# Kernel tuning notes

Measured on AMD Instinct MI355X. Metric: run time of the kernel, lower is better.

Reference implementation:

```python
import jax, jax.numpy as jnp
import numpy as np

N = 50000
H = 4
C = 32  # hidden_channels // heads
NEG_SLOPE = 0.2


def gat_layer(x, W, a_src, a_dst, b, src, dst):
    # x: [N, F_in]; W: [F_in, H*C]; a_src/a_dst: [H, C]; b: [H*C]
    h = (x @ W).reshape(N, H, C)                      # [N, H, C]
    alpha_src = jnp.sum(h * a_src, axis=-1)           # [N, H]
    alpha_dst = jnp.sum(h * a_dst, axis=-1)           # [N, H]
    e = jax.nn.leaky_relu(alpha_src[src] + alpha_dst[dst], NEG_SLOPE)  # [E, H]
    # softmax over incoming edges per destination node (stable)
    m = jax.ops.segment_max(e, dst, num_segments=N)   # [N, H]
    p = jnp.exp(e - m[dst])                           # [E, H]
    s = jax.ops.segment_sum(p, dst, num_segments=N)   # [N, H]
    alpha = p / s[dst]                                # [E, H]
    msg = h[src] * alpha[:, :, None]                  # [E, H, C]
    out = jax.ops.segment_sum(msg, dst, num_segments=N)  # [N, H, C]
    return out.reshape(N, H * C) + b


def setup_inputs() -> dict:
    key = jax.random.key(0)
    ks = jax.random.split(key, 12)
    E = 1600000
    x = jax.random.normal(ks[0], (N, 128), dtype=jnp.float32)
    edge_index = jax.random.randint(ks[1], (2, E), 0, N, dtype=jnp.int32)
    s = 0.08
    return {
        "x": x,
        "edge_index": edge_index,
        "W1": jax.random.normal(ks[2], (128, H * C), dtype=jnp.float32) * s,
        "a_src1": jax.random.normal(ks[3], (H, C), dtype=jnp.float32) * s,
        "a_dst1": jax.random.normal(ks[4], (H, C), dtype=jnp.float32) * s,
        "b1": jnp.zeros((H * C,), dtype=jnp.float32),
        "W2": jax.random.normal(ks[5], (H * C, H * C), dtype=jnp.float32) * s,
        "a_src2": jax.random.normal(ks[6], (H, C), dtype=jnp.float32) * s,
        "a_dst2": jax.random.normal(ks[7], (H, C), dtype=jnp.float32) * s,
        "b2": jnp.zeros((H * C,), dtype=jnp.float32),
    }


def reference(x, edge_index, W1, a_src1, a_dst1, b1, W2, a_src2, a_dst2, b2):
    # PyG GATConv default add_self_loops=True: append (i -> i) edges
    loops = jnp.arange(N, dtype=edge_index.dtype)
    src = jnp.concatenate([edge_index[0], loops])
    dst = jnp.concatenate([edge_index[1], loops])
    # layer 1 + ELU (dropout is identity in eval mode)
    h = gat_layer(x, W1, a_src1, a_dst1, b1, src, dst)
    h = jax.nn.elu(h)
    # layer 2 + ELU
    h = gat_layer(h, W2, a_src2, a_dst2, b2, src, dst)
    h = jax.nn.elu(h)
    return h
```

## Files before the change

### kernel.cpp

```cpp
#include <hip/hip_runtime.h>
#include <hip/hip_bf16.h>

static __device__ __forceinline__ float bf2f_lo(unsigned u) {
    return __uint_as_float(u << 16);
}
static __device__ __forceinline__ float bf2f_hi(unsigned u) {
    return __uint_as_float(u & 0xffff0000u);
}
static __device__ __forceinline__ unsigned f2bf_rne_bits(float f) {
    unsigned u = __float_as_uint(f);
    return u + 0x7fffu + ((u >> 16) & 1u);
}
static __device__ __forceinline__ unsigned pack_bf2(float a, float b) {
    return (f2bf_rne_bits(a) >> 16) | (f2bf_rne_bits(b) & 0xffff0000u);
}
static __device__ __forceinline__ float pfun(float e) {
    e = fmaxf(e, 0.2f * e);
    return __expf(e);
}

#define CHUNK 4096

__global__ void kb_zero(int* bucketCount, int NBK) {
    int i = blockIdx.x * 256 + threadIdx.x;
    if (i < NBK) bucketCount[i] = 0;
}

__global__ void kb_count(const int* __restrict__ dst, int* bucketCount,
                         int E, int T, int NBK) {
    __shared__ int cnt[256];
    const int tid = threadIdx.x;
    const int beg = blockIdx.x * CHUNK;
    const int end = min(beg + CHUNK, T);
    cnt[tid] = 0;
    __syncthreads();
    for (int i = beg + tid; i < end; i += 256) {
        int d = (i < E) ? dst[i] : (i - E);
        atomicAdd(&cnt[d >> 8], 1);
    }
    __syncthreads();
    if (tid < NBK && cnt[tid] > 0) atomicAdd(&bucketCount[tid], cnt[tid]);
}

__global__ void kb_scan(const int* __restrict__ bucketCount, int* bucketBase,
                        int* bucketCursor, int* row_ptr, int NBK, int N, int total) {
    __shared__ int sm[256];
    const int tid = threadIdx.x;
    int v = (tid < NBK) ? bucketCount[tid] : 0;
    sm[tid] = v;
    __syncthreads();
    for (int off = 1; off < 256; off <<= 1) {
        int t = (tid >= off) ? sm[tid - off] : 0;
        __syncthreads();
        sm[tid] += t;
        __syncthreads();
    }
    if (tid < NBK) {
        int ex = sm[tid] - v;
        bucketBase[tid] = ex;
        bucketCursor[tid] = ex;
    }
    if (tid == 0) {
        bucketBase[NBK] = total;
        row_ptr[N] = total;
    }
}

__global__ void kb_place(const int* __restrict__ src, const int* __restrict__ dst,
                         int* bucketCursor, unsigned* __restrict__ barr,
                         int E, int T, int NBK) {
    __shared__ int cnt[256];
    __shared__ int wb[256];
    const int tid = threadIdx.x;
    const int beg = blockIdx.x * CHUNK;
    const int end = min(beg + CHUNK, T);
    cnt[tid] = 0;
    __syncthreads();
    for (int i = beg + tid; i < end; i += 256) {
        int d = (i < E) ? dst[i] : (i - E);
        atomicAdd(&cnt[d >> 8], 1);
    }
    __syncthreads();
    if (tid < NBK) {
        int c = cnt[tid];
        wb[tid] = (c > 0) ? atomicAdd(&bucketCursor[tid], c) : 0;
    }
    __syncthreads();
    cnt[tid] = 0;
    __syncthreads();
    for (int i = beg + tid; i < end; i += 256) {
        int s, d;
        if (i < E) { s = src[i]; d = dst[i]; }
        else       { s = i - E;  d = s; }
        int g = d >> 8;
        unsigned pk = (unsigned)s | ((unsigned)(d & 255) << 16);
        int r = atomicAdd(&cnt[g], 1);
        barr[wb[g] + r] = pk;
    }
}

__global__ void kb_csr(const unsigned* __restrict__ barr, const int* __restrict__ bucketBase,
                       int* __restrict__ row_ptr, int* __restrict__ col, int N) {
    __shared__ int cnt[256];
    __shared__ int sm[256];
    __shared__ int cur[256];
    const int tid = threadIdx.x;
    const int b = blockIdx.x;
    const int beg = bucketBase[b];
    const int end = bucketBase[b + 1];
    cnt[tid] = 0;
    __syncthreads();
    for (int i = beg + tid; i < end; i += 256)
        atomicAdd(&cnt[barr[i] >> 16], 1);
    __syncthreads();
    int v = cnt[tid];
    sm[tid] = v;
    __syncthreads();
    for (int off = 1; off < 256; off <<= 1) {
        int t = (tid >= off) ? sm[tid - off] : 0;
        __syncthreads();
        sm[tid] += t;
        __syncthreads();
    }
    int ex = sm[tid] - v;
    int n = b * 256 + tid;
    if (n < N) row_ptr[n] = beg + ex;
    cur[tid] = beg + ex;
    __syncthreads();
    for (int i = beg + tid; i < end; i += 256) {
        unsigned p = barr[i];
        int pos = atomicAdd(&cur[p >> 16], 1);
        col[pos] = (int)(p & 0xFFFFu);
    }
}

#define KC 32
__launch_bounds__(512, 1)
__global__ void k_gemm(const float* __restrict__ A, const float* __restrict__ W,
                       const float* __restrict__ a_src, const float* __restrict__ a_dst,
                       unsigned* __restrict__ Hout,
                       float* __restrict__ asrc_o, float* __restrict__ adst_o,
                       int nrows) {
    __shared__ float Wl[KC * 128];
    __shared__ float Xl[128 * (KC + 4)];
    const int tid = threadIdx.x;
    const int tx = tid & 15;
    const int ty = tid >> 4;
    const int row0 = blockIdx.x * 128;

    float acc[4][8];
#pragma unroll
    for (int i = 0; i < 4; i++)
#pragma unroll
        for (int j = 0; j < 8; j++) acc[i][j] = 0.f;

    for (int kc = 0; kc < 128; kc += KC) {
#pragma unroll
        for (int it = 0; it < 2; ++it) {
            int ff = it * 512 + tid;
            int r = ff >> 5, cq = ff & 31;
            *(float4*)&Wl[r * 128 + cq * 4] = *(const float4*)&W[(size_t)(kc + r) * 128 + cq * 4];
        }
#pragma unroll
        for (int it = 0; it < 2; ++it) {
            int ff = it * 512 + tid;
            int r = ff >> 3, kq = ff & 7;
            int gr = row0 + r;
            float4 v = make_float4(0.f, 0.f, 0.f, 0.f);
            if (gr < nrows) v = *(const float4*)&A[(size_t)gr * 128 + kc + kq * 4];
            *(float4*)&Xl[r * (KC + 4) + kq * 4] = v;
        }
        __syncthreads();
#pragma unroll
        for (int k0 = 0; k0 < KC; k0 += 4) {
            float4 xv[4];
#pragma unroll
            for (int i = 0; i < 4; i++)
                xv[i] = *(float4*)&Xl[(4 * ty + i) * (KC + 4) + k0];
            const float* xp = (const float*)xv;
#pragma unroll
            for (int kk = 0; kk < 4; ++kk) {
                float4 w0 = *(float4*)&Wl[(k0 + kk) * 128 + 8 * tx];
                float4 w1 = *(float4*)&Wl[(k0 + kk) * 128 + 8 * tx + 4];
#pragma unroll
                for (int i = 0; i < 4; i++) {
                    float xs = xp[i * 4 + kk];
                    acc[i][0] += xs * w0.x; acc[i][1] += xs * w0.y;
                    acc[i][2] += xs * w0.z; acc[i][3] += xs * w0.w;
                    acc[i][4] += xs * w1.x; acc[i][5] += xs * w1.y;
                    acc[i][6] += xs * w1.z; acc[i][7] += xs * w1.w;
                }
            }
        }
        __syncthreads();
    }

    const int head = tx >> 2;
    const int c0 = 8 * tx;
    float as_c[8], ad_c[8];
#pragma unroll
    for (int j = 0; j < 8; j++) { as_c[j] = a_src[c0 + j]; ad_c[j] = a_dst[c0 + j]; }
#pragma unroll
    for (int i = 0; i < 4; i++) {
        int gr = row0 + 4 * ty + i;
        float ps = 0.f, pd = 0.f;
#pragma unroll
        for (int j = 0; j < 8; j++) { ps += acc[i][j] * as_c[j]; pd += acc[i][j] * ad_c[j]; }
        ps += __shfl_xor(ps, 1); ps += __shfl_xor(ps, 2);
        pd += __shfl_xor(pd, 1); pd += __shfl_xor(pd, 2);
        if (gr < nrows) {
            if ((tx & 3) == 0) {
                asrc_o[(size_t)gr * 4 + head] = ps;
                adst_o[(size_t)gr * 4 + head] = pd;
            }
            uint4 o;
            o.x = pack_bf2(acc[i][0], acc[i][1]);
            o.y = pack_bf2(acc[i][2], acc[i][3]);
            o.z = pack_bf2(acc[i][4], acc[i][5]);
            o.w = pack_bf2(acc[i][6], acc[i][7]);
            *(uint4*)&Hout[(size_t)gr * 64 + 4 * tx] = o;
        }
    }
}

#define BAT 16
__launch_bounds__(256)
__global__ void k_aggr(const unsigned* __restrict__ h,
                       const float* __restrict__ asrc, const float* __restrict__ adst,
                       const float* __restrict__ bias,
                       const int* __restrict__ row_ptr, const int* __restrict__ col,
                       float* __restrict__ out, int N) {
    const int lane = threadIdx.x & 63;
    const int d = blockIdx.x * 4 + (threadIdx.x >> 6);
    if (d >= N) return;
    const int eb  = lane >> 2;
    const int hp  = lane & 3;
    const int hdc = lane >> 4;
    const float adv = adst[(size_t)d * 4 + hp];
    const int beg = row_ptr[d];
    const int end = row_ptr[d + 1];

    float ac0 = 0.f, ac1 = 0.f, sp = 0.f;

    int cv = 0;
    { int idx = beg + eb; if (idx < end) cv = col[idx]; }

    for (int j = beg; j < end; j += BAT) {
        int cvn = 0;
        { int idx = j + BAT + eb; if (idx < end) cvn = col[idx]; }

        float a = asrc[(size_t)(unsigned)cv * 4 + hp];
        float p = (j + eb < end) ? pfun(a + adv) : 0.f;
        sp += p;

        unsigned u[BAT];
#pragma unroll
        for (int k = 0; k < BAT; ++k) {
            int sk = __builtin_amdgcn_readlane(cv, 4 * k);
            u[k] = h[(size_t)(unsigned)sk * 64 + lane];
        }
#pragma unroll
        for (int k = 0; k < BAT; ++k) {
            float pk = __shfl(p, 4 * k + hdc);
            ac0 += pk * bf2f_lo(u[k]);
            ac1 += pk * bf2f_hi(u[k]);
        }
        cv = cvn;
    }

    sp += __shfl_xor(sp, 4);
    sp += __shfl_xor(sp, 8);
    sp += __shfl_xor(sp, 16);
    sp += __shfl_xor(sp, 32);
    float spv = __shfl(sp, hdc);
    float inv = 1.f / spv;

    int c = 2 * lane;
    float v0 = ac0 * inv + bias[c];
    float v1 = ac1 * inv + bias[c + 1];
    v0 = (v0 > 0.f) ? v0 : (__expf(v0) - 1.f);
    v1 = (v1 > 0.f) ? v1 : (__expf(v1) - 1.f);
    *(float2*)&out[(size_t)d * 128 + c] = make_float2(v0, v1);
}

extern "C" void kernel_launch(void* const* d_in, const int* in_sizes, int n_in,
                              void* d_out, int out_size, void* d_ws, size_t ws_size,
                              hipStream_t stream) {
    const float* x      = (const float*)d_in[0];
    const int*   ei     = (const int*)d_in[1];
    const float* W1     = (const float*)d_in[2];
    const float* a_src1 = (const float*)d_in[3];
    const float* a_dst1 = (const float*)d_in[4];
    const float* b1     = (const float*)d_in[5];
    const float* W2     = (const float*)d_in[6];
    const float* a_src2 = (const float*)d_in[7];
    const float* a_dst2 = (const float*)d_in[8];
    const float* b2     = (const float*)d_in[9];

    const int N = in_sizes[0] / 128;
    const int E = in_sizes[1] / 2;
    const int T = E + N;
    const int NBK = (N + 255) / 256;
    const int* src = ei;
    const int* dst = ei + E;

    char* w = (char*)d_ws;
    auto alloc = [&](size_t bytes) -> char* {
        char* p = w;
        w += (bytes + 255) & ~(size_t)255;
        return p;
    };
    unsigned* h_bf    = (unsigned*)alloc((size_t)N * 64 * 4);
    float*    o1      = (float*)alloc((size_t)N * 128 * 4);
    float*    asrc    = (float*)alloc((size_t)N * 4 * 4);
    float*    adst    = (float*)alloc((size_t)N * 4 * 4);
    int*      row_ptr = (int*)alloc((size_t)(N + 1) * 4);
    int*      col     = (int*)alloc((size_t)T * 4);
    int*      bCount  = (int*)alloc((size_t)NBK * 4);
    int*      bBase   = (int*)alloc((size_t)(NBK + 1) * 4);
    int*      bCursor = (int*)alloc((size_t)NBK * 4);
    unsigned* barr    = (unsigned*)o1;
    (void)ws_size; (void)n_in; (void)out_size;

    const int PB = (T + CHUNK - 1) / CHUNK;

    hipLaunchKernelGGL(kb_zero, dim3((NBK + 255) / 256), dim3(256), 0, stream, bCount, NBK);
    hipLaunchKernelGGL(kb_count, dim3(PB), dim3(256), 0, stream, dst, bCount, E, T, NBK);
    hipLaunchKernelGGL(kb_scan, dim3(1), dim3(256), 0, stream, bCount, bBase, bCursor, row_ptr, NBK, N, T);
    hipLaunchKernelGGL(kb_place, dim3(PB), dim3(256), 0, stream, src, dst, bCursor, barr, E, T, NBK);
    hipLaunchKernelGGL(kb_csr, dim3(NBK), dim3(256), 0, stream, barr, bBase, row_ptr, col, N);

    const int GB = (N + 127) / 128;
    const int AB = (N + 3) / 4;

    hipLaunchKernelGGL(k_gemm, dim3(GB), dim3(512), 0, stream, x, W1, a_src1, a_dst1, h_bf, asrc, adst, N);
    hipLaunchKernelGGL(k_aggr, dim3(AB), dim3(256), 0, stream, h_bf, asrc, adst, b1, row_ptr, col, o1, N);
    hipLaunchKernelGGL(k_gemm, dim3(GB), dim3(512), 0, stream, o1, W2, a_src2, a_dst2, h_bf, asrc, adst, N);
    hipLaunchKernelGGL(k_aggr, dim3(AB), dim3(256), 0, stream, h_bf, asrc, adst, b2, row_ptr, col, (float*)d_out, N);
}
```

Before: 329.2 us.

## Rewrite node projection GEMM with fp16 MFMA and persistent waves

Replaces the fp32 SIMT tiled GEMM with a kernel that converts W to fp16 once per block, keeps the weight fragments in registers, and runs 16x16x32 f16 MFMA instructions over 16-row tiles in a persistent grid-stride loop. Attention logits are computed from the MFMA accumulators with cross-lane shuffles. The aim is to cut the GEMM's ALU cost and its shared-memory staging. It gives up precision by converting inputs and weights to fp16, and the large register-resident weight set may limit occupancy.

New measurement: 307.0 us. -6.7%, faster.

```diff
diff --git a/kernel.cpp b/kernel.cpp
--- a/kernel.cpp
+++ b/kernel.cpp
@@ -1,5 +1,8 @@
 #include <hip/hip_runtime.h>
 #include <hip/hip_bf16.h>
+
+typedef _Float16 half8 __attribute__((ext_vector_type(8)));
+typedef float f32x4 __attribute__((ext_vector_type(4)));
 
 static __device__ __forceinline__ float bf2f_lo(unsigned u) {
     return __uint_as_float(u << 16);
@@ -134,91 +137,84 @@
     }
 }
 
-#define KC 32
-__launch_bounds__(512, 1)
+__launch_bounds__(256)
 __global__ void k_gemm(const float* __restrict__ A, const float* __restrict__ W,
                        const float* __restrict__ a_src, const float* __restrict__ a_dst,
                        unsigned* __restrict__ Hout,
                        float* __restrict__ asrc_o, float* __restrict__ adst_o,
-                       int nrows) {
-    __shared__ float Wl[KC * 128];
-    __shared__ float Xl[128 * (KC + 4)];
-    const int tid = threadIdx.x;
-    const int tx = tid & 15;
-    const int ty = tid >> 4;
-    const int row0 = blockIdx.x * 128;
-
-    float acc[4][8];
-#pragma unroll
-    for (int i = 0; i < 4; i++)
-#pragma unroll
-        for (int j = 0; j < 8; j++) acc[i][j] = 0.f;
-
-    for (int kc = 0; kc < 128; kc += KC) {
-#pragma unroll
-        for (int it = 0; it < 2; ++it) {
-            int ff = it * 512 + tid;
-            int r = ff >> 5, cq = ff & 31;
-            *(float4*)&Wl[r * 128 + cq * 4] = *(const float4*)&W[(size_t)(kc + r) * 128 + cq * 4];
-        }
-#pragma unroll
-        for (int it = 0; it < 2; ++it) {
-            int ff = it * 512 + tid;
-            int r = ff >> 3, kq = ff & 7;
-            int gr = row0 + r;
-            float4 v = make_float4(0.f, 0.f, 0.f, 0.f);
-            if (gr < nrows) v = *(const float4*)&A[(size_t)gr * 128 + kc + kq * 4];
-            *(float4*)&Xl[r * (KC + 4) + kq * 4] = v;
-        }
-        __syncthreads();
-#pragma unroll
-        for (int k0 = 0; k0 < KC; k0 += 4) {
-            float4 xv[4];
-#pragma unroll
-            for (int i = 0; i < 4; i++)
-                xv[i] = *(float4*)&Xl[(4 * ty + i) * (KC + 4) + k0];
-            const float* xp = (const float*)xv;
-#pragma unroll
-            for (int kk = 0; kk < 4; ++kk) {
-                float4 w0 = *(float4*)&Wl[(k0 + kk) * 128 + 8 * tx];
-                float4 w1 = *(float4*)&Wl[(k0 + kk) * 128 + 8 * tx + 4];
-#pragma unroll
-                for (int i = 0; i < 4; i++) {
-                    float xs = xp[i * 4 + kk];
-                    acc[i][0] += xs * w0.x; acc[i][1] += xs * w0.y;
-                    acc[i][2] += xs * w0.z; acc[i][3] += xs * w0.w;
-                    acc[i][4] += xs * w1.x; acc[i][5] += xs * w1.y;
-                    acc[i][6] += xs * w1.z; acc[i][7] += xs * w1.w;
-                }
+                       int nrows, int ntiles) {
+    __shared__ _Float16 Wt[128 * 136];
+    const int tid = threadIdx.x;
+    for (int idx = tid; idx < 128 * 128 / 4; idx += 256) {
+        int k = idx >> 5;
+        int c4 = (idx & 31) * 4;
+        float4 v = *(const float4*)&W[(size_t)k * 128 + c4];
+        Wt[(c4 + 0) * 136 + k] = (_Float16)v.x;
+        Wt[(c4 + 1) * 136 + k] = (_Float16)v.y;
+        Wt[(c4 + 2) * 136 + k] = (_Float16)v.z;
+        Wt[(c4 + 3) * 136 + k] = (_Float16)v.w;
+    }
+    __syncthreads();
+    const int lane = tid & 63;
+    const int m = lane & 15, quad = lane >> 4;
+
+    half8 wf[4][8];
+#pragma unroll
+    for (int ks = 0; ks < 4; ++ks)
+#pragma unroll
+        for (int ct = 0; ct < 8; ++ct)
+            wf[ks][ct] = *(half8*)&Wt[(ct * 16 + m) * 136 + ks * 32 + quad * 8];
+
+    const int wv = (blockIdx.x * 256 + tid) >> 6;
+    const int nwaves = gridDim.x * 4;
+    for (int t = wv; t < ntiles; t += nwaves) {
+        const int row = t * 16 + m;
+        const int rc = min(row, nrows - 1);
+        const float* ap = A + (size_t)rc * 128;
+        f32x4 acc[8];
+#pragma unroll
+        for (int ct = 0; ct < 8; ++ct) acc[ct] = (f32x4){0.f, 0.f, 0.f, 0.f};
+#pragma unroll
+        for (int ks = 0; ks < 4; ++ks) {
+            float4 x0 = *(const float4*)&ap[ks * 32 + quad * 8];
+            float4 x1 = *(const float4*)&ap[ks * 32 + quad * 8 + 4];
+            half8 af;
+            af[0] = (_Float16)x0.x; af[1] = (_Float16)x0.y;
+            af[2] = (_Float16)x0.z; af[3] = (_Float16)x0.w;
+            af[4] = (_Float16)x1.x; af[5] = (_Float16)x1.y;
+            af[6] = (_Float16)x1.z; af[7] = (_Float16)x1.w;
+#pragma unroll
+            for (int ct = 0; ct < 8; ++ct)
+                acc[ct] = __builtin_amdgcn_mfma_f32_16x16x32_f16(wf[ks][ct], af, acc[ct], 0, 0, 0);
+        }
+        if (row < nrows) {
+#pragma unroll
+            for (int ct = 0; ct < 8; ++ct) {
+                uint2 o;
+                o.x = pack_bf2(acc[ct][0], acc[ct][1]);
+                o.y = pack_bf2(acc[ct][2], acc[ct][3]);
+                *(uint2*)&Hout[(size_t)row * 64 + ct * 8 + quad * 2] = o;
             }
         }
-        __syncthreads();
-    }
-
-    const int head = tx >> 2;
-    const int c0 = 8 * tx;
-    float as_c[8], ad_c[8];
-#pragma unroll
-    for (int j = 0; j < 8; j++) { as_c[j] = a_src[c0 + j]; ad_c[j] = a_dst[c0 + j]; }
-#pragma unroll
-    for (int i = 0; i < 4; i++) {
-        int gr = row0 + 4 * ty + i;
-        float ps = 0.f, pd = 0.f;
-#pragma unroll
-        for (int j = 0; j < 8; j++) { ps += acc[i][j] * as_c[j]; pd += acc[i][j] * ad_c[j]; }
-        ps += __shfl_xor(ps, 1); ps += __shfl_xor(ps, 2);
-        pd += __shfl_xor(pd, 1); pd += __shfl_xor(pd, 2);
-        if (gr < nrows) {
-            if ((tx & 3) == 0) {
-                asrc_o[(size_t)gr * 4 + head] = ps;
-                adst_o[(size_t)gr * 4 + head] = pd;
+        float ps[4] = {0.f, 0.f, 0.f, 0.f}, pd[4] = {0.f, 0.f, 0.f, 0.f};
+#pragma unroll
+        for (int ct = 0; ct < 8; ++ct) {
+            int hh = ct >> 1;
+#pragma unroll
+            for (int r = 0; r < 4; ++r) {
+                int c = ct * 16 + quad * 4 + r;
+                ps[hh] += acc[ct][r] * a_src[c];
+                pd[hh] += acc[ct][r] * a_dst[c];
             }
-            uint4 o;
-            o.x = pack_bf2(acc[i][0], acc[i][1]);
-            o.y = pack_bf2(acc[i][2], acc[i][3]);
-            o.z = pack_bf2(acc[i][4], acc[i][5]);
-            o.w = pack_bf2(acc[i][6], acc[i][7]);
-            *(uint4*)&Hout[(size_t)gr * 64 + 4 * tx] = o;
+        }
+#pragma unroll
+        for (int hh = 0; hh < 4; ++hh) {
+            ps[hh] += __shfl_xor(ps[hh], 16); ps[hh] += __shfl_xor(ps[hh], 32);
+            pd[hh] += __shfl_xor(pd[hh], 16); pd[hh] += __shfl_xor(pd[hh], 32);
+        }
+        if (row < nrows) {
+            asrc_o[(size_t)row * 4 + quad] = ps[quad];
+            adst_o[(size_t)row * 4 + quad] = pd[quad];
         }
     }
 }
@@ -241,7 +237,6 @@
     const int end = row_ptr[d + 1];
 
     float ac0 = 0.f, ac1 = 0.f, sp = 0.f;
-
     int cv = 0;
     { int idx = beg + eb; if (idx < end) cv = col[idx]; }
 
@@ -330,11 +325,12 @@
     hipLaunchKernelGGL(kb_place, dim3(PB), dim3(256), 0, stream, src, dst, bCursor, barr, E, T, NBK);
     hipLaunchKernelGGL(kb_csr, dim3(NBK), dim3(256), 0, stream, barr, bBase, row_ptr, col, N);
 
-    const int GB = (N + 127) / 128;
+    const int ntiles = (N + 15) / 16;
+    const int GB = 512;
     const int AB = (N + 3) / 4;
 
-    hipLaunchKernelGGL(k_gemm, dim3(GB), dim3(512), 0, stream, x, W1, a_src1, a_dst1, h_bf, asrc, adst, N);
+    hipLaunchKernelGGL(k_gemm, dim3(GB), dim3(256), 0, stream, x, W1, a_src1, a_dst1, h_bf, asrc, adst, N, ntiles);
     hipLaunchKernelGGL(k_aggr, dim3(AB), dim3(256), 0, stream, h_bf, asrc, adst, b1, row_ptr, col, o1, N);
-    hipLaunchKernelGGL(k_gemm, dim3(GB), dim3(512), 0, stream, o1, W2, a_src2, a_dst2, h_bf, asrc, adst, N);
+    hipLaunchKernelGGL(k_gemm, dim3(GB), dim3(256), 0, stream, o1, W2, a_src2, a_dst2, h_bf, asrc, adst, N, ntiles);
     hipLaunchKernelGGL(k_aggr, dim3(AB), dim3(256), 0, stream, h_bf, asrc, adst, b2, row_ptr, col, (float*)d_out, N);
 }
```
